# Optimization experiments

Measured on AMD Instinct MI355X. Metric: run time of the kernel, lower is better.

Reference implementation:

```python
import jax, jax.numpy as jnp
import numpy as np

WEIGHT_SCALE = 0.01      # weight_scale buffer
WEIGHT_ZP = 8            # weight_zero_point buffer
BIAS_SCALE = 0.01 * 0.047  # bias_scale = weight_scale * activation_scale (from_float)
OUT_FEATURES = 4096
IN_FEATURES = 4096


def setup_inputs() -> dict:
    key = jax.random.key(0)
    k1, k2, k3 = jax.random.split(key, 3)
    x = jax.random.normal(k1, (8, 2048, IN_FEATURES), dtype=jnp.float32)
    # packed uint8 bytes, two 4-bit weights per byte; stored as int32 (values 0..255)
    packed_weight = jax.random.randint(k2, (OUT_FEATURES, IN_FEATURES // 2), 0, 256, dtype=jnp.int32)
    quantized_bias = jax.random.randint(k3, (OUT_FEATURES,), -500, 500, dtype=jnp.int32)
    return {"x": x, "packed_weight": packed_weight, "quantized_bias": quantized_bias}


def _dequantize_weights(packed_weight):
    # low nibble -> even input column, high nibble -> odd input column
    low = packed_weight & 15          # [O, I/2]
    high = (packed_weight >> 4) & 15  # [O, I/2]
    q = jnp.stack([low, high], axis=-1).reshape(OUT_FEATURES, IN_FEATURES)
    return WEIGHT_SCALE * (q.astype(jnp.float32) - WEIGHT_ZP)


def reference(x, packed_weight, quantized_bias):
    W = _dequantize_weights(packed_weight)                 # [O, I]
    b = BIAS_SCALE * quantized_bias.astype(jnp.float32)    # [O]
    # F.linear: x @ W.T + b
    return jnp.einsum('bsi,oi->bso', x, W) + b
```

## Files before the change

### kernel.cpp

```cpp
#include <hip/hip_runtime.h>


typedef __bf16 bf16x8 __attribute__((ext_vector_type(8)));
typedef float f32x4 __attribute__((ext_vector_type(4)));
typedef unsigned short u16;
typedef u16 u16x4 __attribute__((ext_vector_type(4)));
typedef u16 u16x8 __attribute__((ext_vector_type(8)));

static constexpr int Kdim = 4096;
static constexpr int Ndim = 4096;
static constexpr int BM = 256, BN = 256, BK = 64;
static constexpr int NKT = Kdim / BK;
static constexpr int TBUF = BM * BK;

__device__ __forceinline__ u16 f2bf(float f) {
  union { float f; unsigned u; } c; c.f = f;
  unsigned u = c.u;
  return (u16)((u + 0x7FFFu + ((u >> 16) & 1u)) >> 16);
}

__global__ __launch_bounds__(256) void cvt_x_kernel(const float* __restrict__ x,
                                                    u16* __restrict__ xb, int n4) {
  int stride = gridDim.x * blockDim.x;
  for (int i = blockIdx.x * blockDim.x + threadIdx.x; i < n4; i += stride) {
    float4 v = reinterpret_cast<const float4*>(x)[i];
    u16x4 o;
    o.x = f2bf(v.x); o.y = f2bf(v.y); o.z = f2bf(v.z); o.w = f2bf(v.w);
    reinterpret_cast<u16x4*>(xb)[i] = o;
  }
}

__global__ __launch_bounds__(256) void dequant_w_kernel(const int* __restrict__ pw,
                                                        u16* __restrict__ wb, int n4) {
  int stride = gridDim.x * blockDim.x;
  for (int i = blockIdx.x * blockDim.x + threadIdx.x; i < n4; i += stride) {
    int4 v = reinterpret_cast<const int4*>(pw)[i];
    int a[4] = {v.x, v.y, v.z, v.w};
    u16x8 o;
#pragma unroll
    for (int j = 0; j < 4; ++j) {
      o[2 * j]     = f2bf((float)((a[j] & 15) - 8));
      o[2 * j + 1] = f2bf((float)(((a[j] >> 4) & 15) - 8));
    }
    reinterpret_cast<u16x8*>(wb)[i] = o;
  }
}

__device__ __forceinline__ void gload16(const u16* g, const u16* l) {
  __builtin_amdgcn_global_load_lds(
      (const __attribute__((address_space(1))) void*)g,
      (__attribute__((address_space(3))) void*)l,
      16, 0, 0);
}

__global__ __launch_bounds__(512, 2) void gemm_kernel(const u16* __restrict__ A,
                                                      const u16* __restrict__ B,
                                                      const int* __restrict__ qbias,
                                                      float* __restrict__ C,
                                                      int Ntiles) {
  extern __shared__ u16 smem[];
  u16* As = smem;
  u16* Bs = smem + 3 * TBUF;

  const int tid = threadIdx.x;
  const int lane = tid & 63;
  const int wave = tid >> 6;
  const int wm = wave >> 2, wn = wave & 3;

  const int cpx = gridDim.x >> 3;
  const int bid = blockIdx.x;
  const int swz = (bid & 7) * cpx + (bid >> 3);
  const int bx = swz % Ntiles;
  const int by = swz / Ntiles;
  const int m0 = by * BM, n0 = bx * BN;

  const int srow = tid >> 3;
  const int fcol = (((tid & 7) ^ (srow & 7)) << 3);
  const u16* pa[4];
  const u16* pb[4];
#pragma unroll
  for (int i = 0; i < 4; ++i) {
    pa[i] = A + (size_t)(m0 + i * 64 + srow) * Kdim + fcol;
    pb[i] = B + (size_t)(n0 + i * 64 + srow) * Kdim + fcol;
  }
  const int wbase = (tid & 0x1C0) * 8;

  const int e0 = ((lane >> 4) ^ (lane & 7)) << 3;
  const int e1 = e0 ^ 32;
  const int arow = (wm * 128 + (lane & 15)) * 64;
  const int brow = (wn * 64 + (lane & 15)) * 64;

  f32x4 acc[8][4] = {};

#pragma unroll
  for (int i = 0; i < 4; ++i) gload16(pb[i], Bs + i * 4096 + wbase);
#pragma unroll
  for (int i = 0; i < 4; ++i) gload16(pa[i], As + i * 4096 + wbase);
#pragma unroll
  for (int i = 0; i < 4; ++i) gload16(pa[i] + BK, As + TBUF + i * 4096 + wbase);
  asm volatile("s_waitcnt vmcnt(4)" ::: "memory");
  __builtin_amdgcn_s_barrier();

  int rbuf = 0;
  for (int t = 0; t < NKT; ++t) {
    const u16* aL = As + rbuf * TBUF;
    const u16* bL = Bs + (t & 1) * TBUF;
    const u16* aW = As + ((rbuf + 2) % 3) * TBUF;
    const u16* bW = Bs + ((t + 1) & 1) * TBUF;
    const bool stb = (t + 1) < NKT;
    const bool sta = (t + 2) < NKT;
    const int kob = (t + 1) * BK;
    const int koa = (t + 2) * BK;

    bf16x8 af[4], bf[4][2];

#define PHASE_TAIL(ACC_BASE, KH)                                              \
    __builtin_amdgcn_s_barrier();                                             \
    asm volatile("s_waitcnt lgkmcnt(0)" ::: "memory");                        \
    __builtin_amdgcn_sched_barrier(0);                                        \
    __builtin_amdgcn_s_setprio(1);                                            \
    _Pragma("unroll")                                                         \
    for (int m = 0; m < 4; ++m)                                               \
      _Pragma("unroll")                                                       \
      for (int n = 0; n < 4; ++n)                                             \
        acc[(ACC_BASE) + m][n] = __builtin_amdgcn_mfma_f32_16x16x32_bf16(     \
            af[m], bf[n][KH], acc[(ACC_BASE) + m][n], 0, 0, 0);               \
    __builtin_amdgcn_s_setprio(0);                                            \
    __builtin_amdgcn_sched_barrier(0);                                        \
    __builtin_amdgcn_s_barrier();

#pragma unroll
    for (int m = 0; m < 4; ++m)
      af[m] = *(const bf16x8*)(aL + arow + m * 1024 + e0);
#pragma unroll
    for (int n = 0; n < 4; ++n) {
      bf[n][0] = *(const bf16x8*)(bL + brow + n * 1024 + e0);
      bf[n][1] = *(const bf16x8*)(bL + brow + n * 1024 + e1);
    }
    if (stb) { gload16(pb[0] + kob, bW + 0 * 4096 + wbase);
               gload16(pb[1] + kob, bW + 1 * 4096 + wbase); }
    PHASE_TAIL(0, 0)

#pragma unroll
    for (int m = 0; m < 4; ++m)
      af[m] = *(const bf16x8*)(aL + arow + m * 1024 + e1);
    if (stb) { gload16(pb[2] + kob, bW + 2 * 4096 + wbase);
               gload16(pb[3] + kob, bW + 3 * 4096 + wbase); }
    PHASE_TAIL(0, 1)

#pragma unroll
    for (int m = 0; m < 4; ++m)
      af[m] = *(const bf16x8*)(aL + arow + 4096 + m * 1024 + e0);
    if (sta) { gload16(pa[0] + koa, aW + 0 * 4096 + wbase);
               gload16(pa[1] + koa, aW + 1 * 4096 + wbase); }
    PHASE_TAIL(4, 0)

#pragma unroll
    for (int m = 0; m < 4; ++m)
      af[m] = *(const bf16x8*)(aL + arow + 4096 + m * 1024 + e1);
    if (sta) { gload16(pa[2] + koa, aW + 2 * 4096 + wbase);
               gload16(pa[3] + koa, aW + 3 * 4096 + wbase); }
    __builtin_amdgcn_s_barrier();
    asm volatile("s_waitcnt lgkmcnt(0)" ::: "memory");
    __builtin_amdgcn_sched_barrier(0);
    __builtin_amdgcn_s_setprio(1);
#pragma unroll
    for (int m = 0; m < 4; ++m)
#pragma unroll
      for (int n = 0; n < 4; ++n)
        acc[4 + m][n] = __builtin_amdgcn_mfma_f32_16x16x32_bf16(
            af[m], bf[n][1], acc[4 + m][n], 0, 0, 0);
    __builtin_amdgcn_s_setprio(0);
    __builtin_amdgcn_sched_barrier(0);

    if (sta)      asm volatile("s_waitcnt vmcnt(4)" ::: "memory");
    else if (stb) asm volatile("s_waitcnt vmcnt(0)" ::: "memory");
    __builtin_amdgcn_s_barrier();

    rbuf = (rbuf == 2) ? 0 : rbuf + 1;
#undef PHASE_TAIL
  }

  const float wscale = 0.01f;
  const float bscale = (float)(0.01 * 0.047);
  const int col0 = n0 + wn * 64 + (lane & 15);
  const int row0 = m0 + wm * 128 + ((lane >> 4) << 2);
#pragma unroll
  for (int n = 0; n < 4; ++n) {
    const int col = col0 + n * 16;
    const float bias = bscale * (float)qbias[col];
#pragma unroll
    for (int m = 0; m < 8; ++m) {
      const int rr = row0 + m * 16;
#pragma unroll
      for (int j = 0; j < 4; ++j)
        C[(size_t)(rr + j) * Ndim + col] = wscale * acc[m][n][j] + bias;
    }
  }
}

extern "C" void kernel_launch(void* const* d_in, const int* in_sizes, int n_in,
                              void* d_out, int out_size, void* d_ws, size_t ws_size,
                              hipStream_t stream) {
  const float* x  = (const float*)d_in[0];
  const int*   pw = (const int*)d_in[1];
  const int*   qb = (const int*)d_in[2];
  float* out = (float*)d_out;

  const int M = in_sizes[0] / Kdim;

  u16* xb = (u16*)d_ws;
  u16* wb = (u16*)((char*)d_ws + (size_t)M * Kdim * 2);

  cvt_x_kernel<<<2048, 256, 0, stream>>>(x, xb, M * Kdim / 4);
  dequant_w_kernel<<<1024, 256, 0, stream>>>(pw, wb, Ndim * Kdim / 8);

  const int Ntiles = Ndim / BN;
  const int nwg = (M / BM) * Ntiles;
  static const size_t lds_bytes = 5u * TBUF * sizeof(u16);
  (void)hipFuncSetAttribute((const void*)gemm_kernel,
                            hipFuncAttributeMaxDynamicSharedMemorySize,
                            (int)lds_bytes);
  gemm_kernel<<<nwg, 512, lds_bytes, stream>>>(xb, wb, qb, out, Ntiles);
}
```

Measured before the change: 550.4 us.

## Load B operand straight into registers, drop B LDS staging and per-phase barriers

The weight (B) tile now goes from global memory directly into a register double buffer (bq0/bq1) per lane, instead of being staged through LDS. This removes the B LDS buffers and cuts the A/B ring to four A buffers, with one workgroup barrier per K-tile instead of one per phase. The goal is to save LDS traffic and barrier stalls. In exchange, B global reads are less coalesced, waves that share wn fetch the same rows again, and register pressure rises under launch_bounds(512,2), which risks spills.

```diff
diff --git a/kernel.cpp b/kernel.cpp
--- a/kernel.cpp
+++ b/kernel.cpp
@@ -60,7 +60,6 @@
                                                       int Ntiles) {
   extern __shared__ u16 smem[];
   u16* As = smem;
-  u16* Bs = smem + 3 * TBUF;
 
   const int tid = threadIdx.x;
   const int lane = tid & 63;
@@ -77,23 +76,24 @@
   const int srow = tid >> 3;
   const int fcol = (((tid & 7) ^ (srow & 7)) << 3);
   const u16* pa[4];
-  const u16* pb[4];
-#pragma unroll
-  for (int i = 0; i < 4; ++i) {
+#pragma unroll
+  for (int i = 0; i < 4; ++i)
     pa[i] = A + (size_t)(m0 + i * 64 + srow) * Kdim + fcol;
-    pb[i] = B + (size_t)(n0 + i * 64 + srow) * Kdim + fcol;
-  }
+  const u16* pblane = B + (size_t)(n0 + wn * 64 + (lane & 15)) * Kdim + ((lane >> 4) * 8);
   const int wbase = (tid & 0x1C0) * 8;
 
   const int e0 = ((lane >> 4) ^ (lane & 7)) << 3;
   const int e1 = e0 ^ 32;
   const int arow = (wm * 128 + (lane & 15)) * 64;
-  const int brow = (wn * 64 + (lane & 15)) * 64;
 
   f32x4 acc[8][4] = {};
-
-#pragma unroll
-  for (int i = 0; i < 4; ++i) gload16(pb[i], Bs + i * 4096 + wbase);
+  bf16x8 bq0[4][2], bq1[4][2];
+
+#pragma unroll
+  for (int n = 0; n < 4; ++n) {
+    bq0[n][0] = *(const bf16x8*)(pblane + (size_t)n * 16 * Kdim);
+    bq0[n][1] = *(const bf16x8*)(pblane + (size_t)n * 16 * Kdim + 32);
+  }
 #pragma unroll
   for (int i = 0; i < 4; ++i) gload16(pa[i], As + i * 4096 + wbase);
 #pragma unroll
@@ -101,21 +101,19 @@
   asm volatile("s_waitcnt vmcnt(4)" ::: "memory");
   __builtin_amdgcn_s_barrier();
 
-  int rbuf = 0;
-  for (int t = 0; t < NKT; ++t) {
-    const u16* aL = As + rbuf * TBUF;
-    const u16* bL = Bs + (t & 1) * TBUF;
-    const u16* aW = As + ((rbuf + 2) % 3) * TBUF;
-    const u16* bW = Bs + ((t + 1) & 1) * TBUF;
-    const bool stb = (t + 1) < NKT;
-    const bool sta = (t + 2) < NKT;
-    const int kob = (t + 1) * BK;
-    const int koa = (t + 2) * BK;
-
-    bf16x8 af[4], bf[4][2];
-
-#define PHASE_TAIL(ACC_BASE, KH)                                              \
-    __builtin_amdgcn_s_barrier();                                             \
+#define MFMAS(ACC_BASE, AF, BQ, KH)                                           \
+    asm volatile("s_waitcnt lgkmcnt(4)" ::: "memory");                        \
+    __builtin_amdgcn_sched_barrier(0);                                        \
+    __builtin_amdgcn_s_setprio(1);                                            \
+    _Pragma("unroll")                                                         \
+    for (int m = 0; m < 4; ++m)                                               \
+      _Pragma("unroll")                                                       \
+      for (int n = 0; n < 4; ++n)                                             \
+        acc[(ACC_BASE) + m][n] = __builtin_amdgcn_mfma_f32_16x16x32_bf16(     \
+            AF[m], BQ[n][KH], acc[(ACC_BASE) + m][n], 0, 0, 0);               \
+    __builtin_amdgcn_s_setprio(0);
+
+#define MFMAS0(ACC_BASE, AF, BQ, KH)                                          \
     asm volatile("s_waitcnt lgkmcnt(0)" ::: "memory");                        \
     __builtin_amdgcn_sched_barrier(0);                                        \
     __builtin_amdgcn_s_setprio(1);                                            \
@@ -124,62 +122,67 @@
       _Pragma("unroll")                                                       \
       for (int n = 0; n < 4; ++n)                                             \
         acc[(ACC_BASE) + m][n] = __builtin_amdgcn_mfma_f32_16x16x32_bf16(     \
-            af[m], bf[n][KH], acc[(ACC_BASE) + m][n], 0, 0, 0);               \
-    __builtin_amdgcn_s_setprio(0);                                            \
+            AF[m], BQ[n][KH], acc[(ACC_BASE) + m][n], 0, 0, 0);               \
+    __builtin_amdgcn_s_setprio(0);
+
+#define TILE(T, BQ_CUR, BQ_NXT)                                               \
+  {                                                                           \
+    const int t = (T);                                                        \
+    const u16* aL = As + (t & 3) * TBUF;                                      \
+    const u16* aW = As + ((t + 2) & 3) * TBUF;                                \
+    const bool stb = (t + 1) < NKT;                                           \
+    const bool sta = (t + 2) < NKT;                                           \
+    const int kob = (t + 1) * BK;                                             \
+    const int koa = (t + 2) * BK;                                             \
+    bf16x8 a0[4], a1[4];                                                      \
+    _Pragma("unroll")                                                         \
+    for (int m = 0; m < 4; ++m)                                               \
+      a0[m] = *(const bf16x8*)(aL + arow + m * 1024 + e0);                    \
+                     \
+    _Pragma("unroll")                                                         \
+    for (int m = 0; m < 4; ++m)                                               \
+      a1[m] = *(const bf16x8*)(aL + arow + 4096 + m * 1024 + e0);             \
+    if (stb) {                                                                \
+      _Pragma("unroll")                                                       \
+      for (int n = 0; n < 4; ++n)                                             \
+        BQ_NXT[n][0] = *(const bf16x8*)(pblane + (size_t)n * 16 * Kdim + kob);\
+    }                                                                         \
+    MFMAS(0, a0, BQ_CUR, 0)                                                   \
+                    \
+    _Pragma("unroll")                                                         \
+    for (int m = 0; m < 4; ++m)                                               \
+      a0[m] = *(const bf16x8*)(aL + arow + m * 1024 + e1);                    \
+    if (stb) {                                                                \
+      _Pragma("unroll")                                                       \
+      for (int n = 0; n < 4; ++n)                                             \
+        BQ_NXT[n][1] = *(const bf16x8*)(pblane + (size_t)n * 16 * Kdim + kob + 32);\
+    }                                                                         \
+    MFMAS(4, a1, BQ_CUR, 0)                                                   \
+                    \
+    _Pragma("unroll")                                                         \
+    for (int m = 0; m < 4; ++m)                                               \
+      a1[m] = *(const bf16x8*)(aL + arow + 4096 + m * 1024 + e1);             \
+    if (sta) { gload16(pa[0] + koa, aW + 0 * 4096 + wbase);                   \
+               gload16(pa[1] + koa, aW + 1 * 4096 + wbase); }                 \
+    MFMAS(0, a0, BQ_CUR, 1)                                                   \
+                                       \
+    if (sta) { gload16(pa[2] + koa, aW + 2 * 4096 + wbase);                   \
+               gload16(pa[3] + koa, aW + 3 * 4096 + wbase); }                 \
+    MFMAS0(4, a1, BQ_CUR, 1)                                                  \
     __builtin_amdgcn_sched_barrier(0);                                        \
-    __builtin_amdgcn_s_barrier();
-
-#pragma unroll
-    for (int m = 0; m < 4; ++m)
-      af[m] = *(const bf16x8*)(aL + arow + m * 1024 + e0);
-#pragma unroll
-    for (int n = 0; n < 4; ++n) {
-      bf[n][0] = *(const bf16x8*)(bL + brow + n * 1024 + e0);
-      bf[n][1] = *(const bf16x8*)(bL + brow + n * 1024 + e1);
-    }
-    if (stb) { gload16(pb[0] + kob, bW + 0 * 4096 + wbase);
-               gload16(pb[1] + kob, bW + 1 * 4096 + wbase); }
-    PHASE_TAIL(0, 0)
-
-#pragma unroll
-    for (int m = 0; m < 4; ++m)
-      af[m] = *(const bf16x8*)(aL + arow + m * 1024 + e1);
-    if (stb) { gload16(pb[2] + kob, bW + 2 * 4096 + wbase);
-               gload16(pb[3] + kob, bW + 3 * 4096 + wbase); }
-    PHASE_TAIL(0, 1)
-
-#pragma unroll
-    for (int m = 0; m < 4; ++m)
-      af[m] = *(const bf16x8*)(aL + arow + 4096 + m * 1024 + e0);
-    if (sta) { gload16(pa[0] + koa, aW + 0 * 4096 + wbase);
-               gload16(pa[1] + koa, aW + 1 * 4096 + wbase); }
-    PHASE_TAIL(4, 0)
-
-#pragma unroll
-    for (int m = 0; m < 4; ++m)
-      af[m] = *(const bf16x8*)(aL + arow + 4096 + m * 1024 + e1);
-    if (sta) { gload16(pa[2] + koa, aW + 2 * 4096 + wbase);
-               gload16(pa[3] + koa, aW + 3 * 4096 + wbase); }
-    __builtin_amdgcn_s_barrier();
-    asm volatile("s_waitcnt lgkmcnt(0)" ::: "memory");
-    __builtin_amdgcn_sched_barrier(0);
-    __builtin_amdgcn_s_setprio(1);
-#pragma unroll
-    for (int m = 0; m < 4; ++m)
-#pragma unroll
-      for (int n = 0; n < 4; ++n)
-        acc[4 + m][n] = __builtin_amdgcn_mfma_f32_16x16x32_bf16(
-            af[m], bf[n][1], acc[4 + m][n], 0, 0, 0);
-    __builtin_amdgcn_s_setprio(0);
-    __builtin_amdgcn_sched_barrier(0);
-
-    if (sta)      asm volatile("s_waitcnt vmcnt(4)" ::: "memory");
-    else if (stb) asm volatile("s_waitcnt vmcnt(0)" ::: "memory");
-    __builtin_amdgcn_s_barrier();
-
-    rbuf = (rbuf == 2) ? 0 : rbuf + 1;
-#undef PHASE_TAIL
-  }
+       \
+    if (sta)      { asm volatile("s_waitcnt vmcnt(4)" ::: "memory"); }        \
+    else if (stb) { asm volatile("s_waitcnt vmcnt(0)" ::: "memory"); }        \
+    __builtin_amdgcn_s_barrier();                                             \
+  }
+
+  for (int j = 0; j < NKT / 2; ++j) {
+    TILE(2 * j,     bq0, bq1)
+    TILE(2 * j + 1, bq1, bq0)
+  }
+#undef TILE
+#undef MFMAS
+#undef MFMAS0
 
   const float wscale = 0.01f;
   const float bscale = (float)(0.01 * 0.047);
@@ -217,7 +220,7 @@
 
   const int Ntiles = Ndim / BN;
   const int nwg = (M / BM) * Ntiles;
-  static const size_t lds_bytes = 5u * TBUF * sizeof(u16);
+  static const size_t lds_bytes = 4u * TBUF * sizeof(u16);
   (void)hipFuncSetAttribute((const void*)gemm_kernel,
                             hipFuncAttributeMaxDynamicSharedMemorySize,
                             (int)lds_bytes);
```

Measured after the change: 794.7 us. 1.44x slower.

## Load B fragments directly into registers and drop LDS staging for weights

Applied to the files above, without the earlier changes.

The weight operand is no longer staged through LDS. Each wave loads its B fragments straight from global memory into registers one K-step ahead, and only A goes through LDS, now with a 4-deep buffer. The per-phase barriers are replaced by finer lgkmcnt/vmcnt waits, cutting LDS traffic and synchronisation. The cost is that B is re-read from global/L2 by every wave sharing the same columns (wm=0 and wm=1), with uncoalesced 16-byte per-lane reads, plus more register pressure. The B register reload may also race with MFMAs still using the old values unless the compiler orders them.

```diff
diff --git a/kernel.cpp b/kernel.cpp
--- a/kernel.cpp
+++ b/kernel.cpp
@@ -60,7 +60,6 @@
                                                       int Ntiles) {
   extern __shared__ u16 smem[];
   u16* As = smem;
-  u16* Bs = smem + 3 * TBUF;
 
   const int tid = threadIdx.x;
   const int lane = tid & 63;
@@ -77,23 +76,24 @@
   const int srow = tid >> 3;
   const int fcol = (((tid & 7) ^ (srow & 7)) << 3);
   const u16* pa[4];
-  const u16* pb[4];
-#pragma unroll
-  for (int i = 0; i < 4; ++i) {
+#pragma unroll
+  for (int i = 0; i < 4; ++i)
     pa[i] = A + (size_t)(m0 + i * 64 + srow) * Kdim + fcol;
-    pb[i] = B + (size_t)(n0 + i * 64 + srow) * Kdim + fcol;
-  }
+  const u16* pblane = B + (size_t)(n0 + wn * 64 + (lane & 15)) * Kdim + ((lane >> 4) * 8);
   const int wbase = (tid & 0x1C0) * 8;
 
   const int e0 = ((lane >> 4) ^ (lane & 7)) << 3;
   const int e1 = e0 ^ 32;
   const int arow = (wm * 128 + (lane & 15)) * 64;
-  const int brow = (wn * 64 + (lane & 15)) * 64;
 
   f32x4 acc[8][4] = {};
-
-#pragma unroll
-  for (int i = 0; i < 4; ++i) gload16(pb[i], Bs + i * 4096 + wbase);
+  bf16x8 bq[4][2];
+
+#pragma unroll
+  for (int n = 0; n < 4; ++n) {
+    bq[n][0] = *(const bf16x8*)(pblane + (size_t)n * 16 * Kdim);
+    bq[n][1] = *(const bf16x8*)(pblane + (size_t)n * 16 * Kdim + 32);
+  }
 #pragma unroll
   for (int i = 0; i < 4; ++i) gload16(pa[i], As + i * 4096 + wbase);
 #pragma unroll
@@ -101,22 +101,7 @@
   asm volatile("s_waitcnt vmcnt(4)" ::: "memory");
   __builtin_amdgcn_s_barrier();
 
-  int rbuf = 0;
-  for (int t = 0; t < NKT; ++t) {
-    const u16* aL = As + rbuf * TBUF;
-    const u16* bL = Bs + (t & 1) * TBUF;
-    const u16* aW = As + ((rbuf + 2) % 3) * TBUF;
-    const u16* bW = Bs + ((t + 1) & 1) * TBUF;
-    const bool stb = (t + 1) < NKT;
-    const bool sta = (t + 2) < NKT;
-    const int kob = (t + 1) * BK;
-    const int koa = (t + 2) * BK;
-
-    bf16x8 af[4], bf[4][2];
-
-#define PHASE_TAIL(ACC_BASE, KH)                                              \
-    __builtin_amdgcn_s_barrier();                                             \
-    asm volatile("s_waitcnt lgkmcnt(0)" ::: "memory");                        \
+#define MFMA16(ACC_BASE, AF, KH)                                              \
     __builtin_amdgcn_sched_barrier(0);                                        \
     __builtin_amdgcn_s_setprio(1);                                            \
     _Pragma("unroll")                                                         \
@@ -124,62 +109,68 @@
       _Pragma("unroll")                                                       \
       for (int n = 0; n < 4; ++n)                                             \
         acc[(ACC_BASE) + m][n] = __builtin_amdgcn_mfma_f32_16x16x32_bf16(     \
-            af[m], bf[n][KH], acc[(ACC_BASE) + m][n], 0, 0, 0);               \
-    __builtin_amdgcn_s_setprio(0);                                            \
-    __builtin_amdgcn_sched_barrier(0);                                        \
+            AF[m], bq[n][KH], acc[(ACC_BASE) + m][n], 0, 0, 0);               \
+    __builtin_amdgcn_s_setprio(0);
+
+  for (int t = 0; t < NKT; ++t) {
+    const u16* aL = As + (t & 3) * TBUF;
+    const u16* aW = As + ((t + 2) & 3) * TBUF;
+    const bool stb = (t + 1) < NKT;
+    const bool sta = (t + 2) < NKT;
+    const int kob = (t + 1) * BK;
+    const int koa = (t + 2) * BK;
+
+    bf16x8 a0[4], a1[4];
+
+#pragma unroll
+    for (int m = 0; m < 4; ++m)
+      a0[m] = *(const bf16x8*)(aL + arow + m * 1024 + e0);
+
+#pragma unroll
+    for (int m = 0; m < 4; ++m)
+      a1[m] = *(const bf16x8*)(aL + arow + 4096 + m * 1024 + e0);
+    asm volatile("s_waitcnt lgkmcnt(4)" ::: "memory");
+    MFMA16(0, a0, 0)
+
+#pragma unroll
+    for (int m = 0; m < 4; ++m)
+      a0[m] = *(const bf16x8*)(aL + arow + m * 1024 + e1);
+    asm volatile("s_waitcnt lgkmcnt(4)" ::: "memory");
+    MFMA16(4, a1, 0)
+
+#pragma unroll
+    for (int m = 0; m < 4; ++m)
+      a1[m] = *(const bf16x8*)(aL + arow + 4096 + m * 1024 + e1);
+    if (stb) {
+#pragma unroll
+      for (int n = 0; n < 4; ++n)
+        bq[n][0] = *(const bf16x8*)(pblane + (size_t)n * 16 * Kdim + kob);
+    }
+    asm volatile("s_waitcnt vmcnt(8)" ::: "memory");
+    asm volatile("s_waitcnt lgkmcnt(4)" ::: "memory");
+    MFMA16(0, a0, 1)
+
+    asm volatile("s_waitcnt lgkmcnt(0)" ::: "memory");
+    MFMA16(4, a1, 1)
+    __builtin_amdgcn_sched_barrier(0);
+    if (stb) {
+#pragma unroll
+      for (int n = 0; n < 4; ++n)
+        bq[n][1] = *(const bf16x8*)(pblane + (size_t)n * 16 * Kdim + kob + 32);
+    }
+    if (sta) {
+      gload16(pa[0] + koa, aW + 0 * 4096 + wbase);
+      gload16(pa[1] + koa, aW + 1 * 4096 + wbase);
+      gload16(pa[2] + koa, aW + 2 * 4096 + wbase);
+      gload16(pa[3] + koa, aW + 3 * 4096 + wbase);
+    }
+    __builtin_amdgcn_sched_barrier(0);
+
+    if (sta)      { asm volatile("s_waitcnt vmcnt(8)" ::: "memory"); }
+    else if (stb) { asm volatile("s_waitcnt vmcnt(0)" ::: "memory"); }
     __builtin_amdgcn_s_barrier();
-
-#pragma unroll
-    for (int m = 0; m < 4; ++m)
-      af[m] = *(const bf16x8*)(aL + arow + m * 1024 + e0);
-#pragma unroll
-    for (int n = 0; n < 4; ++n) {
-      bf[n][0] = *(const bf16x8*)(bL + brow + n * 1024 + e0);
-      bf[n][1] = *(const bf16x8*)(bL + brow + n * 1024 + e1);
-    }
-    if (stb) { gload16(pb[0] + kob, bW + 0 * 4096 + wbase);
-               gload16(pb[1] + kob, bW + 1 * 4096 + wbase); }
-    PHASE_TAIL(0, 0)
-
-#pragma unroll
-    for (int m = 0; m < 4; ++m)
-      af[m] = *(const bf16x8*)(aL + arow + m * 1024 + e1);
-    if (stb) { gload16(pb[2] + kob, bW + 2 * 4096 + wbase);
-               gload16(pb[3] + kob, bW + 3 * 4096 + wbase); }
-    PHASE_TAIL(0, 1)
-
-#pragma unroll
-    for (int m = 0; m < 4; ++m)
-      af[m] = *(const bf16x8*)(aL + arow + 4096 + m * 1024 + e0);
-    if (sta) { gload16(pa[0] + koa, aW + 0 * 4096 + wbase);
-               gload16(pa[1] + koa, aW + 1 * 4096 + wbase); }
-    PHASE_TAIL(4, 0)
-
-#pragma unroll
-    for (int m = 0; m < 4; ++m)
-      af[m] = *(const bf16x8*)(aL + arow + 4096 + m * 1024 + e1);
-    if (sta) { gload16(pa[2] + koa, aW + 2 * 4096 + wbase);
-               gload16(pa[3] + koa, aW + 3 * 4096 + wbase); }
-    __builtin_amdgcn_s_barrier();
-    asm volatile("s_waitcnt lgkmcnt(0)" ::: "memory");
-    __builtin_amdgcn_sched_barrier(0);
-    __builtin_amdgcn_s_setprio(1);
-#pragma unroll
-    for (int m = 0; m < 4; ++m)
-#pragma unroll
-      for (int n = 0; n < 4; ++n)
-        acc[4 + m][n] = __builtin_amdgcn_mfma_f32_16x16x32_bf16(
-            af[m], bf[n][1], acc[4 + m][n], 0, 0, 0);
-    __builtin_amdgcn_s_setprio(0);
-    __builtin_amdgcn_sched_barrier(0);
-
-    if (sta)      asm volatile("s_waitcnt vmcnt(4)" ::: "memory");
-    else if (stb) asm volatile("s_waitcnt vmcnt(0)" ::: "memory");
-    __builtin_amdgcn_s_barrier();
-
-    rbuf = (rbuf == 2) ? 0 : rbuf + 1;
-#undef PHASE_TAIL
-  }
+  }
+#undef MFMA16
 
   const float wscale = 0.01f;
   const float bscale = (float)(0.01 * 0.047);
@@ -217,7 +208,7 @@
 
   const int Ntiles = Ndim / BN;
   const int nwg = (M / BM) * Ntiles;
-  static const size_t lds_bytes = 5u * TBUF * sizeof(u16);
+  static const size_t lds_bytes = 4u * TBUF * sizeof(u16);
   (void)hipFuncSetAttribute((const void*)gemm_kernel,
                             hipFuncAttributeMaxDynamicSharedMemorySize,
                             (int)lds_bytes);
```

Result: slower. 734.6 us (+33.5%).
